# Performance work log

Measured on AMD Instinct MI355X. Metric: run time of the kernel, lower is better.

## Reference

```python
import jax, jax.numpy as jnp
import numpy as np

BN_EPS = 1e-5
TAU = 1.0

def _conv(x, w, pad, groups=1):
    return jax.lax.conv_general_dilated(
        x, w, (1, 1), [(pad, pad), (pad, pad)],
        feature_group_count=groups,
        dimension_numbers=('NCHW', 'OIHW', 'NCHW'))

def _bn(x, p):
    # p: (4, C) rows = gamma, beta, running_mean, running_var (eval-mode BN)
    g, b, m, v = p[0], p[1], p[2], p[3]
    scale = g * jax.lax.rsqrt(v + BN_EPS)
    shift = b - m * scale
    return x * scale[None, :, None, None] + shift[None, :, None, None]

def _dsconv(x, dw, bn1, pw, bn2, pad):
    c = x.shape[1]
    h = jax.nn.silu(_bn(_conv(x, dw, pad, groups=c), bn1))
    return jax.nn.silu(_bn(_conv(h, pw, 0), bn2))

def _make_bn(key, ch):
    k1, k2, k3, k4 = jax.random.split(key, 4)
    g = 1.0 + 0.1 * jax.random.normal(k1, (ch,), jnp.float32)
    b = 0.1 * jax.random.normal(k2, (ch,), jnp.float32)
    m = 0.1 * jax.random.normal(k3, (ch,), jnp.float32)
    v = 0.5 + jax.random.uniform(k4, (ch,), jnp.float32)
    return jnp.stack([g, b, m, v])

def setup_inputs() -> dict:
    key = jax.random.key(0)
    ks = jax.random.split(key, 18)
    B, C, H, W = 4, 256, 128, 128
    P, K = 64, 8
    inp = {
        'x':      jax.random.normal(ks[0], (B, C, H, W), jnp.float32),
        'fp_w1':  0.05 * jax.random.normal(ks[1], (P, C, 1, 1), jnp.float32),
        'fp_bn1': _make_bn(ks[2], P),
        'fp_dw':  0.2 * jax.random.normal(ks[3], (P, 1, 3, 3), jnp.float32),
        'fp_bn2': _make_bn(ks[4], P),
        'protos': jax.random.normal(ks[5], (K, P), jnp.float32),
        'bs_dw':  0.2 * jax.random.normal(ks[6], (1, 1, 3, 3), jnp.float32),
        'bs_bn1': _make_bn(ks[7], 1),
        'bs_pw':  0.2 * jax.random.normal(ks[8], (8, 1, 1, 1), jnp.float32),
        'bs_bn2': _make_bn(ks[9], 8),
        'bl_dw':  0.2 * jax.random.normal(ks[10], (1, 1, 5, 5), jnp.float32),
        'bl_bn1': _make_bn(ks[11], 1),
        'bl_pw':  0.2 * jax.random.normal(ks[12], (8, 1, 1, 1), jnp.float32),
        'bl_bn2': _make_bn(ks[13], 8),
        'fuse_w': 0.2 * jax.random.normal(ks[14], (1, 16, 1, 1), jnp.float32),
        'fuse_b': 0.1 * jax.random.normal(ks[15], (1,), jnp.float32),
        'gamma':  0.5 * jax.random.normal(ks[16], (1,), jnp.float32),
    }
    return inp

def reference(x, fp_w1, fp_bn1, fp_dw, fp_bn2, protos,
              bs_dw, bs_bn1, bs_pw, bs_bn2,
              bl_dw, bl_bn1, bl_pw, bl_bn2,
              fuse_w, fuse_b, gamma):
    # feature_proj: 1x1 conv -> BN -> SiLU -> depthwise 3x3 -> BN -> SiLU
    h = jax.nn.silu(_bn(_conv(x, fp_w1, 0), fp_bn1))
    proj = jax.nn.silu(_bn(_conv(h, fp_dw, 1, groups=fp_dw.shape[0]), fp_bn2))

    # deviation: min L2 distance to K bg prototypes, per-image min-max normalized
    B, P, H, W = proj.shape
    feat = proj.reshape(B, P, H * W).transpose(0, 2, 1)      # (B, HW, P)
    d2 = ((feat * feat).sum(-1, keepdims=True)               # (B, HW, 1)
          + (protos * protos).sum(-1)                        # (K,)
          - 2.0 * jnp.einsum('bnp,kp->bnk', feat, protos))   # (B, HW, K)
    dist = jnp.sqrt(jnp.maximum(d2, 0.0))
    min_dist = dist.min(axis=2) / (TAU + 1e-6)               # (B, HW)
    d_min = min_dist.min(axis=1, keepdims=True)
    d_max = min_dist.max(axis=1, keepdims=True)
    deviation = ((min_dist - d_min) / (d_max - d_min + 1e-6)).reshape(B, 1, H, W)

    # deviation -> attention head: two DS-conv branches (3x3 and 5x5), fuse 1x1, sigmoid
    f1 = _dsconv(deviation, bs_dw, bs_bn1, bs_pw, bs_bn2, pad=1)
    f2 = _dsconv(deviation, bl_dw, bl_bn1, bl_pw, bl_bn2, pad=2)
    attn = jax.nn.sigmoid(_conv(jnp.concatenate([f1, f2], axis=1), fuse_w, 0)
                          + fuse_b[None, :, None, None])
    return x + gamma * (x * attn)
```

## Files before the change

kernel.cpp:

```cpp
#include <hip/hip_runtime.h>
#include <math.h>

#define C_IN 256
#define P_CH 64
#define H_IMG 128
#define W_IMG 128
#define HW (H_IMG*W_IMG)
#define N_IMG 4
#define K_PROTO 8
#define BN_EPS 1e-5f

#define OFF_WT     0
#define OFF_BIASA  16384
#define OFF_PNORM  16448
#define OFF_MINMAX 16456
#define OFF_H      16464
#define OFF_MD     (16464 + 4194304)
#define OFF_ATTN   (OFF_MD + 65536)

__device__ __forceinline__ float silu_f(float x) { return x / (1.f + __expf(-x)); }

__global__ void prep_kernel(const float* __restrict__ w1, const float* __restrict__ bn1,
                            const float* __restrict__ protos, float* __restrict__ ws)
{
    int bx = blockIdx.x, tid = threadIdx.x;
    if (bx < 64) {
        int idx = bx * 256 + tid;
        int c = idx >> 6, p = idx & 63;
        float sc = bn1[p] * rsqrtf(bn1[192 + p] + BN_EPS);
        ws[OFF_WT + idx] = w1[p * C_IN + c] * sc;
    } else {
        if (tid < 64) {
            float sc = bn1[tid] * rsqrtf(bn1[192 + tid] + BN_EPS);
            ws[OFF_BIASA + tid] = bn1[64 + tid] - bn1[128 + tid] * sc;
        }
        if (tid < 8) {
            float s = 0.f;
            for (int p = 0; p < 64; ++p) { float v = protos[tid * 64 + p]; s += v * v; }
            ws[OFF_PNORM + tid] = s;
        }
        if (tid < 4) {
            unsigned* mm = (unsigned*)(ws + OFF_MINMAX);
            mm[tid * 2]     = 0x7f7fffffu;
            mm[tid * 2 + 1] = 0u;
        }
    }
}

__global__ __launch_bounds__(256, 4) void conv1x1_kernel(
    const float* __restrict__ x, const float* __restrict__ wt,
    const float* __restrict__ bias, float* __restrict__ h)
{
    __shared__ float xs[2][8][64];
    int bx = blockIdx.x;
    int img = bx >> 8;
    int rem = bx & 255;
    int row = rem >> 1;
    int half = rem & 1;
    int tid = threadIdx.x;
    int pgrp = tid >> 6;
    int lane = tid & 63;
    int sc_ = tid >> 4;
    int sp_ = (tid & 15) * 4;

    const float* xbase = x + (size_t)img * C_IN * HW + row * W_IMG + half * 64;
    float* hb = h + (size_t)img * P_CH * HW + row * W_IMG + half * 64;

    float acc[16];
#pragma unroll
    for (int j = 0; j < 16; ++j) acc[j] = 0.f;

    if (tid < 128)
        *(float4*)&xs[0][sc_][sp_] = *(const float4*)(xbase + (size_t)sc_ * HW + sp_);
    __syncthreads();

    for (int k = 0; k < 32; ++k) {
        float4 nxt;
        if (k < 31 && tid < 128)
            nxt = *(const float4*)(xbase + (size_t)((k + 1) * 8 + sc_) * HW + sp_);

        const float (*xb)[64] = xs[k & 1];
        int c0 = k * 8;
#pragma unroll
        for (int cl = 0; cl < 8; ++cl) {
            float xv = xb[cl][lane];
            int wof = __builtin_amdgcn_readfirstlane((c0 + cl) * 64 + pgrp * 16);
            const float* w = wt + wof;
#pragma unroll
            for (int j = 0; j < 16; ++j)
                acc[j] = fmaf(xv, w[j], acc[j]);
        }
        if (k < 31 && tid < 128)
            *(float4*)&xs[(k + 1) & 1][sc_][sp_] = nxt;
        __syncthreads();
    }

    int bof = __builtin_amdgcn_readfirstlane(pgrp * 16);
#pragma unroll
    for (int j = 0; j < 16; ++j) {
        int p = bof + j;
        hb[(size_t)p * HW + lane] = silu_f(acc[j] + bias[p]);
    }
}

__global__ __launch_bounds__(1024) void dwconv_dev_kernel(
    const float* __restrict__ h, const float* __restrict__ dw,
    const float* __restrict__ bn2, const float* __restrict__ protos,
    const float* __restrict__ pnorm, float* __restrict__ md,
    unsigned* __restrict__ minmax)
{
    __shared__ float smem[4 * 8 * 324];
    int img = blockIdx.x >> 6;
    int t = blockIdx.x & 63;
    int y0 = (t >> 3) << 4, x0 = (t & 7) << 4;
    int tid = threadIdx.x;
    int q = tid >> 8;
    int qtid = tid & 255;
    int ty = qtid >> 4, tx = qtid & 15;

    const float* himg = h + (size_t)img * P_CH * HW;
    float* qt = smem + q * (8 * 324);

    int  pre_off[11];
    bool pre_ok[11];
    bool pre_v[11];
#pragma unroll
    for (int r = 0; r < 11; ++r) {
        int l = qtid + r * 256;
        bool valid = l < 2592;
        int cl = l / 324;
        int rr = l - cl * 324;
        int ly = rr / 18, lx = rr - ly * 18;
        int yy = y0 - 1 + ly, xx = x0 - 1 + lx;
        bool inb = (yy >= 0) & (yy < H_IMG) & (xx >= 0) & (xx < W_IMG);
        pre_v[r] = valid;
        pre_ok[r] = valid && inb;
        pre_off[r] = cl * HW + (inb ? (yy * W_IMG + xx) : 0);
    }

    float norm2 = 0.f;
    float dot[K_PROTO];
#pragma unroll
    for (int k = 0; k < K_PROTO; ++k) dot[k] = 0.f;

    {
        const float* hs = himg + (size_t)(q * 16) * HW;
#pragma unroll
        for (int r = 0; r < 11; ++r) {
            float v = pre_ok[r] ? hs[pre_off[r]] : 0.f;
            if (pre_v[r]) qt[qtid + r * 256] = v;
        }
    }
    __syncthreads();

    for (int k = 0; k < 2; ++k) {
        float pf[11];
        if (k == 0) {
            const float* hs = himg + (size_t)(q * 16 + 8) * HW;
#pragma unroll
            for (int r = 0; r < 11; ++r)
                pf[r] = pre_ok[r] ? hs[pre_off[r]] : 0.f;
        }

        int c0 = q * 16 + k * 8;
#pragma unroll
        for (int cl = 0; cl < 8; ++cl) {
            int ch = c0 + cl;
            const float* tc = qt + cl * 324;
            const float* wch = dw + ch * 9;
            float s = 0.f;
#pragma unroll
            for (int dy = 0; dy < 3; ++dy)
#pragma unroll
                for (int dx = 0; dx < 3; ++dx)
                    s = fmaf(tc[(ty + dy) * 18 + tx + dx], wch[dy * 3 + dx], s);
            float g = bn2[ch], bb = bn2[64 + ch], m = bn2[128 + ch], vv = bn2[192 + ch];
            float scale = g * rsqrtf(vv + BN_EPS);
            float val = silu_f(scale * s + (bb - m * scale));
            norm2 = fmaf(val, val, norm2);
#pragma unroll
            for (int kk = 0; kk < K_PROTO; ++kk)
                dot[kk] = fmaf(val, protos[kk * 64 + ch], dot[kk]);
        }

        if (k == 0) {
            __syncthreads();
#pragma unroll
            for (int r = 0; r < 11; ++r)
                if (pre_v[r]) qt[qtid + r * 256] = pf[r];
            __syncthreads();
        }
    }
    __syncthreads();

    float* P = smem;
    {
        float* dst = P + (q * 256 + qtid) * 9;
        dst[0] = norm2;
#pragma unroll
        for (int kk = 0; kk < K_PROTO; ++kk) dst[1 + kk] = dot[kk];
    }
    __syncthreads();

    float wmin = 1e30f, wmax = -1e30f, mdv = 0.f;
    if (q == 0) {
        float n2 = 0.f, dd[K_PROTO];
#pragma unroll
        for (int kk = 0; kk < K_PROTO; ++kk) dd[kk] = 0.f;
#pragma unroll
        for (int qq = 0; qq < 4; ++qq) {
            const float* src = P + (qq * 256 + qtid) * 9;
            n2 += src[0];
#pragma unroll
            for (int kk = 0; kk < K_PROTO; ++kk) dd[kk] += src[1 + kk];
        }
        float d2min = 1e30f;
#pragma unroll
        for (int kk = 0; kk < K_PROTO; ++kk)
            d2min = fminf(d2min, n2 + pnorm[kk] - 2.f * dd[kk]);
        mdv = sqrtf(fmaxf(d2min, 0.f)) * (1.f / 1.000001f);
        md[img * HW + (y0 + ty) * W_IMG + (x0 + tx)] = mdv;
        wmin = mdv; wmax = mdv;
#pragma unroll
        for (int d = 32; d > 0; d >>= 1) {
            wmin = fminf(wmin, __shfl_xor(wmin, d));
            wmax = fmaxf(wmax, __shfl_xor(wmax, d));
        }
    }
    __syncthreads();
    if (q == 0 && (qtid & 63) == 0) {
        int wid = qtid >> 6;
        smem[wid * 2]     = wmin;
        smem[wid * 2 + 1] = wmax;
    }
    __syncthreads();
    if (tid == 0) {
        float bmin = fminf(fminf(smem[0], smem[2]), fminf(smem[4], smem[6]));
        float bmax = fmaxf(fmaxf(smem[1], smem[3]), fmaxf(smem[5], smem[7]));
        atomicMin(&minmax[img * 2],     __float_as_uint(bmin));
        atomicMax(&minmax[img * 2 + 1], __float_as_uint(bmax));
    }
}

__global__ __launch_bounds__(256) void attn_kernel(
    const float* __restrict__ md, const unsigned* __restrict__ minmax,
    const float* __restrict__ bs_dw, const float* __restrict__ bs_bn1,
    const float* __restrict__ bs_pw, const float* __restrict__ bs_bn2,
    const float* __restrict__ bl_dw, const float* __restrict__ bl_bn1,
    const float* __restrict__ bl_pw, const float* __restrict__ bl_bn2,
    const float* __restrict__ fuse_w, const float* __restrict__ fuse_b,
    float* __restrict__ attn)
{
    __shared__ float tile[20 * 20];
    int img = blockIdx.x >> 6;
    int t = blockIdx.x & 63;
    int y0 = (t >> 3) << 4, x0 = (t & 7) << 4;
    int tid = threadIdx.x;
    int ty = tid >> 4, tx = tid & 15;

    float fdmin = __uint_as_float(minmax[img * 2]);
    float fdmax = __uint_as_float(minmax[img * 2 + 1]);
    float inv = 1.f / (fdmax - fdmin + 1e-6f);

    const float* mdi = md + img * HW;
    for (int l = tid; l < 400; l += 256) {
        int ly = l / 20, lx = l - ly * 20;
        int yy = y0 - 2 + ly, xx = x0 - 2 + lx;
        float v = 0.f;
        if (yy >= 0 && yy < H_IMG && xx >= 0 && xx < W_IMG)
            v = (mdi[yy * W_IMG + xx] - fdmin) * inv;
        tile[l] = v;
    }
    __syncthreads();

    float c3 = 0.f;
#pragma unroll
    for (int dy = 0; dy < 3; ++dy)
#pragma unroll
        for (int dx = 0; dx < 3; ++dx)
            c3 = fmaf(tile[(ty + 1 + dy) * 20 + tx + 1 + dx], bs_dw[dy * 3 + dx], c3);
    float c5 = 0.f;
#pragma unroll
    for (int dy = 0; dy < 5; ++dy)
#pragma unroll
        for (int dx = 0; dx < 5; ++dx)
            c5 = fmaf(tile[(ty + dy) * 20 + tx + dx], bl_dw[dy * 5 + dx], c5);

    float s1 = bs_bn1[0] * rsqrtf(bs_bn1[3] + BN_EPS);
    float t1 = silu_f(s1 * c3 + (bs_bn1[1] - bs_bn1[2] * s1));
    float s2 = bl_bn1[0] * rsqrtf(bl_bn1[3] + BN_EPS);
    float t2 = silu_f(s2 * c5 + (bl_bn1[1] - bl_bn1[2] * s2));

    float acc = fuse_b[0];
#pragma unroll
    for (int c = 0; c < 8; ++c) {
        float scs = bs_bn2[c] * rsqrtf(bs_bn2[24 + c] + BN_EPS);
        float u1 = silu_f(scs * (bs_pw[c] * t1) + (bs_bn2[8 + c] - bs_bn2[16 + c] * scs));
        acc = fmaf(fuse_w[c], u1, acc);
        float scl = bl_bn2[c] * rsqrtf(bl_bn2[24 + c] + BN_EPS);
        float u2 = silu_f(scl * (bl_pw[c] * t2) + (bl_bn2[8 + c] - bl_bn2[16 + c] * scl));
        acc = fmaf(fuse_w[8 + c], u2, acc);
    }
    float a = 1.f / (1.f + __expf(-acc));
    attn[img * HW + (y0 + ty) * W_IMG + (x0 + tx)] = a;
}

__global__ __launch_bounds__(256) void final_kernel(
    const float* __restrict__ x, const float* __restrict__ attn,
    const float* __restrict__ gamma, float* __restrict__ out)
{
    size_t i = ((size_t)blockIdx.x * 256 + (size_t)threadIdx.x) * 4;
    float g = gamma[0];
    int b = (int)(i / ((size_t)C_IN * HW));
    int hw = (int)(i % HW);
    const float4 xv = *(const float4*)(x + i);
    const float4 av = *(const float4*)(attn + (size_t)b * HW + hw);
    float4 o;
    o.x = xv.x * (1.f + g * av.x);
    o.y = xv.y * (1.f + g * av.y);
    o.z = xv.z * (1.f + g * av.z);
    o.w = xv.w * (1.f + g * av.w);
    *(float4*)(out + i) = o;
}

extern "C" void kernel_launch(void* const* d_in, const int* in_sizes, int n_in,
                              void* d_out, int out_size, void* d_ws, size_t ws_size,
                              hipStream_t stream) {
    const float* x      = (const float*)d_in[0];
    const float* fp_w1  = (const float*)d_in[1];
    const float* fp_bn1 = (const float*)d_in[2];
    const float* fp_dw  = (const float*)d_in[3];
    const float* fp_bn2 = (const float*)d_in[4];
    const float* protos = (const float*)d_in[5];
    const float* bs_dw  = (const float*)d_in[6];
    const float* bs_bn1 = (const float*)d_in[7];
    const float* bs_pw  = (const float*)d_in[8];
    const float* bs_bn2 = (const float*)d_in[9];
    const float* bl_dw  = (const float*)d_in[10];
    const float* bl_bn1 = (const float*)d_in[11];
    const float* bl_pw  = (const float*)d_in[12];
    const float* bl_bn2 = (const float*)d_in[13];
    const float* fuse_w = (const float*)d_in[14];
    const float* fuse_b = (const float*)d_in[15];
    const float* gamma  = (const float*)d_in[16];
    float* ws  = (float*)d_ws;
    float* out = (float*)d_out;

    prep_kernel<<<65, 256, 0, stream>>>(fp_w1, fp_bn1, protos, ws);
    conv1x1_kernel<<<1024, 256, 0, stream>>>(x, ws + OFF_WT, ws + OFF_BIASA, ws + OFF_H);
    dwconv_dev_kernel<<<256, 1024, 0, stream>>>(ws + OFF_H, fp_dw, fp_bn2, protos,
                                                ws + OFF_PNORM, ws + OFF_MD,
                                                (unsigned*)(ws + OFF_MINMAX));
    attn_kernel<<<256, 256, 0, stream>>>(ws + OFF_MD, (const unsigned*)(ws + OFF_MINMAX),
                                         bs_dw, bs_bn1, bs_pw, bs_bn2,
                                         bl_dw, bl_bn1, bl_pw, bl_bn2,
                                         fuse_w, fuse_b, ws + OFF_ATTN);
    final_kernel<<<16384, 256, 0, stream>>>(x, ws + OFF_ATTN, gamma, out);
}
```

Before: 220.5 us.

## Use bf16 MFMA for 1x1 projection conv and store intermediate in bf16

Replaces the FP32 FMA 1x1 convolution with a bf16 MFMA (16x16x32) GEMM per image row. Input channels are converted to bf16 as they are staged into double-buffered LDS, and weights are pre-scaled into bf16 in the prep kernel. The intermediate activation h is now stored as bf16, which halves its write and read traffic into the depthwise kernel. The cost is bf16 rounding of x, weights and h, which may shift the deviation min/max normalization.

```diff
diff --git a/kernel.cpp b/kernel.cpp
--- a/kernel.cpp
+++ b/kernel.cpp
@@ -10,15 +10,29 @@
 #define K_PROTO 8
 #define BN_EPS 1e-5f
 
-#define OFF_WT     0
-#define OFF_BIASA  16384
-#define OFF_PNORM  16448
-#define OFF_MINMAX 16456
-#define OFF_H      16464
-#define OFF_MD     (16464 + 4194304)
+typedef unsigned short u16;
+typedef __attribute__((ext_vector_type(4))) short bf16x4;
+typedef __attribute__((ext_vector_type(8))) short bf16x8;
+typedef __attribute__((ext_vector_type(4))) float f32x4;
+
+#define OFF_WTBF   0
+#define OFF_BIASA  8192
+#define OFF_PNORM  8256
+#define OFF_MINMAX 8264
+#define OFF_H      8272
+#define OFF_MD     (8272 + 2097152)
 #define OFF_ATTN   (OFF_MD + 65536)
 
 __device__ __forceinline__ float silu_f(float x) { return x / (1.f + __expf(-x)); }
+
+__device__ __forceinline__ u16 f2bf(float f) {
+    union { float f; unsigned u; } v; v.f = f;
+    unsigned r = v.u + 0x7fffu + ((v.u >> 16) & 1u);
+    return (u16)(r >> 16);
+}
+__device__ __forceinline__ float bf2f(u16 s) {
+    union { unsigned u; float f; } v; v.u = ((unsigned)s) << 16; return v.f;
+}
 
 __global__ void prep_kernel(const float* __restrict__ w1, const float* __restrict__ bn1,
                             const float* __restrict__ protos, float* __restrict__ ws)
@@ -26,9 +40,9 @@
     int bx = blockIdx.x, tid = threadIdx.x;
     if (bx < 64) {
         int idx = bx * 256 + tid;
-        int c = idx >> 6, p = idx & 63;
-        float sc = bn1[p] * rsqrtf(bn1[192 + p] + BN_EPS);
-        ws[OFF_WT + idx] = w1[p * C_IN + c] * sc;
+        int n = idx >> 8, k = idx & 255;
+        float sc = bn1[n] * rsqrtf(bn1[192 + n] + BN_EPS);
+        ((u16*)(ws + OFF_WTBF))[idx] = f2bf(w1[n * C_IN + k] * sc);
     } else {
         if (tid < 64) {
             float sc = bn1[tid] * rsqrtf(bn1[192 + tid] + BN_EPS);
@@ -47,64 +61,111 @@
     }
 }
 
-__global__ __launch_bounds__(256, 4) void conv1x1_kernel(
-    const float* __restrict__ x, const float* __restrict__ wt,
-    const float* __restrict__ bias, float* __restrict__ h)
+#define LDA 36
+#define LDB 264
+__global__ __launch_bounds__(256) void conv1x1_kernel(
+    const float* __restrict__ x, const u16* __restrict__ wtb,
+    const float* __restrict__ bias, u16* __restrict__ h)
 {
-    __shared__ float xs[2][8][64];
+    __shared__ u16 As[2][128 * LDA];
+    __shared__ u16 Bs[64 * LDB];
     int bx = blockIdx.x;
-    int img = bx >> 8;
-    int rem = bx & 255;
-    int row = rem >> 1;
-    int half = rem & 1;
+    int img = bx >> 7, row = bx & 127;
     int tid = threadIdx.x;
-    int pgrp = tid >> 6;
-    int lane = tid & 63;
-    int sc_ = tid >> 4;
-    int sp_ = (tid & 15) * 4;
-
-    const float* xbase = x + (size_t)img * C_IN * HW + row * W_IMG + half * 64;
-    float* hb = h + (size_t)img * P_CH * HW + row * W_IMG + half * 64;
-
-    float acc[16];
-#pragma unroll
-    for (int j = 0; j < 16; ++j) acc[j] = 0.f;
-
-    if (tid < 128)
-        *(float4*)&xs[0][sc_][sp_] = *(const float4*)(xbase + (size_t)sc_ * HW + sp_);
-    __syncthreads();
-
-    for (int k = 0; k < 32; ++k) {
-        float4 nxt;
-        if (k < 31 && tid < 128)
-            nxt = *(const float4*)(xbase + (size_t)((k + 1) * 8 + sc_) * HW + sp_);
-
-        const float (*xb)[64] = xs[k & 1];
-        int c0 = k * 8;
-#pragma unroll
-        for (int cl = 0; cl < 8; ++cl) {
-            float xv = xb[cl][lane];
-            int wof = __builtin_amdgcn_readfirstlane((c0 + cl) * 64 + pgrp * 16);
-            const float* w = wt + wof;
-#pragma unroll
-            for (int j = 0; j < 16; ++j)
-                acc[j] = fmaf(xv, w[j], acc[j]);
-        }
-        if (k < 31 && tid < 128)
-            *(float4*)&xs[(k + 1) & 1][sc_][sp_] = nxt;
+    int wid = tid >> 6, lane = tid & 63;
+    int mm = lane & 15, kb = lane >> 4;
+
+    {
+        int n = tid >> 2, k0 = (tid & 3) * 64;
+        const u16* src = wtb + n * 256 + k0;
+        u16* dst = Bs + n * LDB + k0;
+#pragma unroll
+        for (int i = 0; i < 64; i += 4)
+            *(ushort4*)(dst + i) = *(const ushort4*)(src + i);
+    }
+
+    int cp = tid >> 4, pg = tid & 15;
+    const float* xbase = x + (size_t)img * C_IN * HW + row * W_IMG;
+    {
+        const float* xc0 = xbase + (size_t)(2 * cp) * HW;
+        const float* xc1 = xc0 + HW;
+#pragma unroll
+        for (int i = 0; i < 8; ++i) {
+            int px = pg + 16 * i;
+            ushort2 pk; pk.x = f2bf(xc0[px]); pk.y = f2bf(xc1[px]);
+            *(ushort2*)(&As[0][px * LDA + 2 * cp]) = pk;
+        }
+    }
+    __syncthreads();
+
+    f32x4 acc[2][4];
+#pragma unroll
+    for (int mt = 0; mt < 2; ++mt)
+#pragma unroll
+        for (int nt = 0; nt < 4; ++nt) acc[mt][nt] = (f32x4){0.f, 0.f, 0.f, 0.f};
+
+    for (int k = 0; k < 8; ++k) {
+        float p0[8], p1[8];
+        if (k < 7) {
+            const float* xc0 = xbase + (size_t)((k + 1) * 32 + 2 * cp) * HW;
+            const float* xc1 = xc0 + HW;
+#pragma unroll
+            for (int i = 0; i < 8; ++i) {
+                int px = pg + 16 * i;
+                p0[i] = xc0[px]; p1[i] = xc1[px];
+            }
+        }
+
+        const u16* Ab = As[k & 1];
+        bf16x8 afrag[2], bfrag[4];
+#pragma unroll
+        for (int mt = 0; mt < 2; ++mt) {
+            const u16* ap = Ab + (wid * 32 + mt * 16 + mm) * LDA + kb * 8;
+            bf16x4 lo = *(const bf16x4*)ap;
+            bf16x4 hi = *(const bf16x4*)(ap + 4);
+            afrag[mt] = __builtin_shufflevector(lo, hi, 0, 1, 2, 3, 4, 5, 6, 7);
+        }
+#pragma unroll
+        for (int nt = 0; nt < 4; ++nt)
+            bfrag[nt] = *(const bf16x8*)(Bs + (nt * 16 + mm) * LDB + k * 32 + kb * 8);
+#pragma unroll
+        for (int mt = 0; mt < 2; ++mt)
+#pragma unroll
+            for (int nt = 0; nt < 4; ++nt)
+                acc[mt][nt] = __builtin_amdgcn_mfma_f32_16x16x32_bf16(
+                    afrag[mt], bfrag[nt], acc[mt][nt], 0, 0, 0);
+
+        if (k < 7) {
+            u16* An = As[(k + 1) & 1];
+#pragma unroll
+            for (int i = 0; i < 8; ++i) {
+                int px = pg + 16 * i;
+                ushort2 pk; pk.x = f2bf(p0[i]); pk.y = f2bf(p1[i]);
+                *(ushort2*)(&An[px * LDA + 2 * cp]) = pk;
+            }
+        }
         __syncthreads();
     }
 
-    int bof = __builtin_amdgcn_readfirstlane(pgrp * 16);
-#pragma unroll
-    for (int j = 0; j < 16; ++j) {
-        int p = bof + j;
-        hb[(size_t)p * HW + lane] = silu_f(acc[j] + bias[p]);
+#pragma unroll
+    for (int mt = 0; mt < 2; ++mt) {
+        int pxb = wid * 32 + mt * 16 + kb * 4;
+#pragma unroll
+        for (int nt = 0; nt < 4; ++nt) {
+            int n = nt * 16 + mm;
+            float bb = bias[n];
+            ushort4 o;
+            o.x = f2bf(silu_f(acc[mt][nt][0] + bb));
+            o.y = f2bf(silu_f(acc[mt][nt][1] + bb));
+            o.z = f2bf(silu_f(acc[mt][nt][2] + bb));
+            o.w = f2bf(silu_f(acc[mt][nt][3] + bb));
+            *(ushort4*)(h + ((size_t)img * P_CH + n) * HW + row * W_IMG + pxb) = o;
+        }
     }
 }
 
 __global__ __launch_bounds__(1024) void dwconv_dev_kernel(
-    const float* __restrict__ h, const float* __restrict__ dw,
+    const u16* __restrict__ h, const float* __restrict__ dw,
     const float* __restrict__ bn2, const float* __restrict__ protos,
     const float* __restrict__ pnorm, float* __restrict__ md,
     unsigned* __restrict__ minmax)
@@ -118,7 +179,7 @@
     int qtid = tid & 255;
     int ty = qtid >> 4, tx = qtid & 15;
 
-    const float* himg = h + (size_t)img * P_CH * HW;
+    const u16* himg = h + (size_t)img * P_CH * HW;
     float* qt = smem + q * (8 * 324);
 
     int  pre_off[11];
@@ -144,10 +205,10 @@
     for (int k = 0; k < K_PROTO; ++k) dot[k] = 0.f;
 
     {
-        const float* hs = himg + (size_t)(q * 16) * HW;
+        const u16* hs = himg + (size_t)(q * 16) * HW;
 #pragma unroll
         for (int r = 0; r < 11; ++r) {
-            float v = pre_ok[r] ? hs[pre_off[r]] : 0.f;
+            float v = pre_ok[r] ? bf2f(hs[pre_off[r]]) : 0.f;
             if (pre_v[r]) qt[qtid + r * 256] = v;
         }
     }
@@ -156,10 +217,10 @@
     for (int k = 0; k < 2; ++k) {
         float pf[11];
         if (k == 0) {
-            const float* hs = himg + (size_t)(q * 16 + 8) * HW;
+            const u16* hs = himg + (size_t)(q * 16 + 8) * HW;
 #pragma unroll
             for (int r = 0; r < 11; ++r)
-                pf[r] = pre_ok[r] ? hs[pre_off[r]] : 0.f;
+                pf[r] = pre_ok[r] ? bf2f(hs[pre_off[r]]) : 0.f;
         }
 
         int c0 = q * 16 + k * 8;
@@ -347,9 +408,10 @@
     float* out = (float*)d_out;
 
     prep_kernel<<<65, 256, 0, stream>>>(fp_w1, fp_bn1, protos, ws);
-    conv1x1_kernel<<<1024, 256, 0, stream>>>(x, ws + OFF_WT, ws + OFF_BIASA, ws + OFF_H);
-    dwconv_dev_kernel<<<256, 1024, 0, stream>>>(ws + OFF_H, fp_dw, fp_bn2, protos,
-                                                ws + OFF_PNORM, ws + OFF_MD,
+    conv1x1_kernel<<<512, 256, 0, stream>>>(x, (const u16*)(ws + OFF_WTBF),
+                                            ws + OFF_BIASA, (u16*)(ws + OFF_H));
+    dwconv_dev_kernel<<<256, 1024, 0, stream>>>((const u16*)(ws + OFF_H), fp_dw, fp_bn2,
+                                                protos, ws + OFF_PNORM, ws + OFF_MD,
                                                 (unsigned*)(ws + OFF_MINMAX));
     attn_kernel<<<256, 256, 0, stream>>>(ws + OFF_MD, (const unsigned*)(ws + OFF_MINMAX),
                                          bs_dw, bs_bn1, bs_pw, bs_bn2,
```

After: 188.9 us. 1.17x faster.
